# Kernel optimization log

Hardware: AMD Instinct MI355X
Metric: run time of the kernel (lower is better)

The kernel has to match this reference:

```python
import jax, jax.numpy as jnp
import numpy as np

N = 8192      # num nodes = feature dim (A is NxN adjacency used as features)
H = 1024      # bottleneck dim
E = 8192      # num edges
PENALTY = 10.0  # scalar buffer from __init__


def setup_inputs() -> dict:
    key = jax.random.key(0)
    ks = jax.random.split(key, 7)
    return {
        "A": jax.random.normal(ks[0], (N, N), dtype=jnp.float32),
        "W1": jax.random.normal(ks[1], (H, N), dtype=jnp.float32) * 0.02,
        "b1": jax.random.normal(ks[2], (H,), dtype=jnp.float32) * 0.02,
        "W2": jax.random.normal(ks[3], (N, H), dtype=jnp.float32) * 0.02,
        "b2": jax.random.normal(ks[4], (N,), dtype=jnp.float32) * 0.02,
        "edges": jax.random.randint(ks[5], (E, 2), 0, N, dtype=jnp.int32),
        "labels": jax.random.randint(ks[6], (E,), 0, 2, dtype=jnp.int32),
    }


def reference(A, W1, b1, W2, b2, edges, labels):
    ni = edges[:, 0]
    nj = edges[:, 1]
    Xi = A[ni]  # [E, N]
    Xj = A[nj]  # [E, N]
    lab = labels.astype(A.dtype)

    layers = [(W1, b1), (W2, b2)]
    Hi, Hj = Xi, Xj
    loss_1 = jnp.zeros((), A.dtype)
    loss_r_per_edge = jnp.zeros((), A.dtype)
    for (W, b) in layers:
        Hi = jax.nn.sigmoid(Hi @ W.T + b)
        Hj = jax.nn.sigmoid(Hj @ W.T + b)
        # per-edge L2 norm of activation diff at this layer, weighted by label
        loss_1 = loss_1 + jnp.sum(jnp.linalg.norm(Hi - Hj, axis=1) * lab)
        # original code appends weight-row-norm sum + bias norm once per (edge, layer)
        loss_r_per_edge = loss_r_per_edge + jnp.sum(jnp.linalg.norm(W, axis=1)) + jnp.linalg.norm(b)
    loss_r = loss_r_per_edge * jnp.asarray(E, A.dtype)

    # reconstruction loss; penalty scales the diff when label >= 1 (scalar => factors out of norm)
    factor = jnp.where(lab >= 1.0, jnp.asarray(PENALTY, A.dtype), jnp.asarray(1.0, A.dtype))
    loss_2 = jnp.sum(factor * (jnp.linalg.norm(Xi - Hi, axis=1) + jnp.linalg.norm(Xj - Hj, axis=1)))

    return loss_1 + loss_2 + loss_r
```

## Files before the change

### kernel.cpp

```cpp
#include <hip/hip_runtime.h>
#include <hip/hip_bf16.h>
#include <stdint.h>

#define N_DIM 8192
#define H_DIM 1024
#define E_DIM 8192
#define PENALTY_F 10.0f
#define WSCALE 16.0f
#define INV_WSCALE 0.0625f

typedef unsigned short u16;
typedef unsigned char u8;
typedef unsigned int u32;
typedef __attribute__((ext_vector_type(4))) float f32x4;
typedef __attribute__((ext_vector_type(2))) float f32x2;
typedef __attribute__((ext_vector_type(4))) int i32x4;
typedef __attribute__((ext_vector_type(8))) int i32x8;

__device__ __forceinline__ u32 pack4_fp8(float a, float b, float c, float d) {
  u32 p = __builtin_amdgcn_cvt_pk_fp8_f32(a, b, 0, false);
  p = __builtin_amdgcn_cvt_pk_fp8_f32(c, d, p, true);
  return p;
}
__device__ __forceinline__ f32x2 unpk_lo(u32 v) {
  return __builtin_amdgcn_cvt_pk_f32_fp8(v, false);
}
__device__ __forceinline__ f32x2 unpk_hi(u32 v) {
  return __builtin_amdgcn_cvt_pk_f32_fp8(v, true);
}

#define GLD16(ldsptr, gptr)                                                     \
  __builtin_amdgcn_global_load_lds(                                             \
      (__attribute__((address_space(1))) void*)(gptr),                          \
      (__attribute__((address_space(3))) void*)(ldsptr), 16, 0, 0)

__device__ __forceinline__ float wave_red(float v) {
  for (int o = 32; o; o >>= 1) v += __shfl_down(v, o, 64);
  return v;
}

__device__ __forceinline__ float block_reduce1(float v) {
  __shared__ float buf[4];
  v = wave_red(v);
  int lane = threadIdx.x & 63, w = threadIdx.x >> 6;
  if (lane == 0) buf[w] = v;
  __syncthreads();
  float r = 0.f;
  if (threadIdx.x == 0) r = buf[0] + buf[1] + buf[2] + buf[3];
  return r;
}

__global__ void convert_f32_fp8(const float* __restrict__ in,
                                u8* __restrict__ out, int n4, float scale) {
  int i = blockIdx.x * blockDim.x + threadIdx.x;
  if (i < n4) {
    float4 v = ((const float4*)in)[i];
    ((u32*)out)[i] =
        pack4_fp8(v.x * scale, v.y * scale, v.z * scale, v.w * scale);
  }
}

__global__ void prep_w(const float* __restrict__ W1,
                       const float* __restrict__ W2,
                       const float* __restrict__ b1,
                       const float* __restrict__ b2, u8* __restrict__ W1_8,
                       u8* __restrict__ W2_8, float* __restrict__ out) {
  const int blk = blockIdx.x;
  if (blk < H_DIM) {
    const float4* row = (const float4*)(W1 + (size_t)blk * N_DIM);
    u32* orow = (u32*)(W1_8 + (size_t)blk * N_DIM);
    float s = 0.f;
#pragma unroll
    for (int t = 0; t < 8; ++t) {
      int i = threadIdx.x + t * 256;
      float4 v = row[i];
      s += v.x * v.x + v.y * v.y + v.z * v.z + v.w * v.w;
      orow[i] = pack4_fp8(v.x * WSCALE, v.y * WSCALE, v.z * WSCALE,
                          v.w * WSCALE);
    }
    s = block_reduce1(s);
    if (threadIdx.x == 0) atomicAdd(out, sqrtf(s) * (float)E_DIM);
  } else if (blk < H_DIM + N_DIM / 4) {
    __shared__ float buf[4];
    const int wave = threadIdx.x >> 6, lane = threadIdx.x & 63;
    const int r = (blk - H_DIM) * 4 + wave;
    const float4* row = (const float4*)(W2 + (size_t)r * H_DIM);
    u32* orow = (u32*)(W2_8 + (size_t)r * H_DIM);
    float s = 0.f;
#pragma unroll
    for (int t = 0; t < 4; ++t) {
      int i = lane + t * 64;
      float4 v = row[i];
      s += v.x * v.x + v.y * v.y + v.z * v.z + v.w * v.w;
      orow[i] = pack4_fp8(v.x * WSCALE, v.y * WSCALE, v.z * WSCALE,
                          v.w * WSCALE);
    }
    s = wave_red(s);
    if (lane == 0) buf[wave] = sqrtf(s);
    __syncthreads();
    if (threadIdx.x == 0)
      atomicAdd(out, (buf[0] + buf[1] + buf[2] + buf[3]) * (float)E_DIM);
  } else if (blk == H_DIM + N_DIM / 4) {
    const float4* row = (const float4*)b1;
    float4 v = row[threadIdx.x];
    float s = v.x * v.x + v.y * v.y + v.z * v.z + v.w * v.w;
    s = block_reduce1(s);
    if (threadIdx.x == 0) atomicAdd(out, sqrtf(s) * (float)E_DIM);
  } else {
    const float4* row = (const float4*)b2;
    float s = 0.f;
#pragma unroll
    for (int t = 0; t < 8; ++t) {
      float4 v = row[threadIdx.x + t * 256];
      s += v.x * v.x + v.y * v.y + v.z * v.z + v.w * v.w;
    }
    s = block_reduce1(s);
    if (threadIdx.x == 0) atomicAdd(out, sqrtf(s) * (float)E_DIM);
  }
}

#define BM 128
#define BN 128
#define BKB 128

__global__ __launch_bounds__(256) void gemm_fp8_sigmoid(
    const u8* __restrict__ Ag,
    const u8* __restrict__ Bg,
    const float* __restrict__ bias,
    u8* __restrict__ Cg,
    float invScale, int K, int Nd) {
  __shared__ __align__(16) u8 Xs[BM * BKB];
  __shared__ __align__(16) u8 Ws[BN * BKB];

  const int tid = threadIdx.x;
  const int wave = tid >> 6, lane = tid & 63;
  const int wr = wave >> 1, wc = wave & 1;
  const size_t rowBase = (size_t)blockIdx.y * BM;
  const size_t colBase = (size_t)blockIdx.x * BN;

  f32x4 acc[4][4] = {};

  const int i8 = lane >> 3;
  const int c8 = lane & 7;
  const int sw = c8 ^ i8;

  const int quad = lane >> 4;
  const int m15 = lane & 15;

  for (int k0 = 0; k0 < K; k0 += BKB) {
#pragma unroll
    for (int j = 0; j < 4; ++j) {
      const int r0 = (wave * 4 + j) * 8;
      const u8* gx = Ag + (rowBase + r0 + i8) * (size_t)K + (k0 + sw * 16);
      GLD16(&Xs[r0 * BKB], gx);
      const u8* gw = Bg + (colBase + r0 + i8) * (size_t)K + (k0 + sw * 16);
      GLD16(&Ws[r0 * BKB], gw);
    }
    __syncthreads();

    i32x8 af[4], bfr[4];
#pragma unroll
    for (int t = 0; t < 4; ++t) {
      const int m = wr * 64 + t * 16 + m15;
      i32x4 alo = *(const i32x4*)&Xs[m * BKB + ((2 * quad) ^ (m & 7)) * 16];
      i32x4 ahi = *(const i32x4*)&Xs[m * BKB + ((2 * quad + 1) ^ (m & 7)) * 16];
      af[t] = __builtin_shufflevector(alo, ahi, 0, 1, 2, 3, 4, 5, 6, 7);
      const int n = wc * 64 + t * 16 + m15;
      i32x4 blo = *(const i32x4*)&Ws[n * BKB + ((2 * quad) ^ (n & 7)) * 16];
      i32x4 bhi = *(const i32x4*)&Ws[n * BKB + ((2 * quad + 1) ^ (n & 7)) * 16];
      bfr[t] = __builtin_shufflevector(blo, bhi, 0, 1, 2, 3, 4, 5, 6, 7);
    }
#pragma unroll
    for (int mt = 0; mt < 4; ++mt)
#pragma unroll
      for (int nt = 0; nt < 4; ++nt)
        acc[mt][nt] = __builtin_amdgcn_mfma_scale_f32_16x16x128_f8f6f4(
            bfr[nt], af[mt], acc[mt][nt], 0, 0,
            0, 0x7F7F7F7F, 0, 0x7F7F7F7F);
    __syncthreads();
  }

  f32x4 bv4[4];
#pragma unroll
  for (int nt = 0; nt < 4; ++nt)
    bv4[nt] = *(const f32x4*)&bias[colBase + wc * 64 + nt * 16 + quad * 4];
#pragma unroll
  for (int mt = 0; mt < 4; ++mt) {
    const size_t grow = rowBase + wr * 64 + mt * 16 + m15;
    u32* crow = (u32*)(Cg + grow * (size_t)Nd + colBase + wc * 64);
#pragma unroll
    for (int nt = 0; nt < 4; ++nt) {
      float v[4];
#pragma unroll
      for (int i = 0; i < 4; ++i) {
        float x = acc[mt][nt][i] * invScale + bv4[nt][i];
        v[i] = WSCALE / (1.0f + __expf(-x));
      }
      crow[nt * 4 + quad] = pack4_fp8(v[0], v[1], v[2], v[3]);
    }
  }
}

__global__ void edge_loss_h(const u8* __restrict__ H1,
                            const int* __restrict__ edges,
                            const int* __restrict__ labels,
                            float* __restrict__ out) {
  __shared__ float buf[4];
  const int wave = threadIdx.x >> 6, lane = threadIdx.x & 63;
  const int e = blockIdx.x * 4 + wave;
  float r = 0.f;
  if (labels[e] != 0) {
    const int ni = edges[e * 2], nj = edges[e * 2 + 1];
    const i32x4 a = ((const i32x4*)(H1 + (size_t)ni * H_DIM))[lane];
    const i32x4 b = ((const i32x4*)(H1 + (size_t)nj * H_DIM))[lane];
    float s = 0.f;
#pragma unroll
    for (int j = 0; j < 4; ++j) {
      f32x2 al = unpk_lo((u32)a[j]), ah = unpk_hi((u32)a[j]);
      f32x2 bl = unpk_lo((u32)b[j]), bh = unpk_hi((u32)b[j]);
      float d0 = al.x - bl.x, d1 = al.y - bl.y;
      float d2 = ah.x - bh.x, d3 = ah.y - bh.y;
      s += d0 * d0 + d1 * d1 + d2 * d2 + d3 * d3;
    }
    s = wave_red(s);
    r = sqrtf(s) * INV_WSCALE;
  }
  if (lane == 0) buf[wave] = r;
  __syncthreads();
  if (threadIdx.x == 0) atomicAdd(out, buf[0] + buf[1] + buf[2] + buf[3]);
}

__global__ void edge_loss_final(const u8* __restrict__ H2,
                                const u8* __restrict__ A8,
                                const int* __restrict__ edges,
                                const int* __restrict__ labels,
                                float* __restrict__ out) {
  __shared__ float buf[4];
  const int wave = threadIdx.x >> 6, lane = threadIdx.x & 63;
  const int e = blockIdx.x * 4 + wave;
  const int ni = edges[e * 2], nj = edges[e * 2 + 1];
  const i32x4* hi = (const i32x4*)(H2 + (size_t)ni * N_DIM);
  const i32x4* hj = (const i32x4*)(H2 + (size_t)nj * N_DIM);
  const i32x4* xi = (const i32x4*)(A8 + (size_t)ni * N_DIM);
  const i32x4* xj = (const i32x4*)(A8 + (size_t)nj * N_DIM);
  float s12 = 0.f, si = 0.f, sj = 0.f;
#pragma unroll 2
  for (int t = 0; t < 8; ++t) {
    const int idx = lane + t * 64;
    i32x4 a = hi[idx], b = hj[idx], x = xi[idx], y = xj[idx];
#pragma unroll
    for (int j = 0; j < 4; ++j) {
      f32x2 al = unpk_lo((u32)a[j]), ah = unpk_hi((u32)a[j]);
      f32x2 bl = unpk_lo((u32)b[j]), bh = unpk_hi((u32)b[j]);
      f32x2 xl = unpk_lo((u32)x[j]), xh = unpk_hi((u32)x[j]);
      f32x2 yl = unpk_lo((u32)y[j]), yh = unpk_hi((u32)y[j]);
      float d;
      d = al.x - bl.x; s12 += d * d;
      d = al.y - bl.y; s12 += d * d;
      d = ah.x - bh.x; s12 += d * d;
      d = ah.y - bh.y; s12 += d * d;
      d = WSCALE * xl.x - al.x; si += d * d;
      d = WSCALE * xl.y - al.y; si += d * d;
      d = WSCALE * xh.x - ah.x; si += d * d;
      d = WSCALE * xh.y - ah.y; si += d * d;
      d = WSCALE * yl.x - bl.x; sj += d * d;
      d = WSCALE * yl.y - bl.y; sj += d * d;
      d = WSCALE * yh.x - bh.x; sj += d * d;
      d = WSCALE * yh.y - bh.y; sj += d * d;
    }
  }
  for (int o = 32; o; o >>= 1) {
    s12 += __shfl_down(s12, o, 64);
    si += __shfl_down(si, o, 64);
    sj += __shfl_down(sj, o, 64);
  }
  if (lane == 0) {
    float lab = (labels[e] != 0) ? 1.f : 0.f;
    float fac = (labels[e] != 0) ? PENALTY_F : 1.f;
    buf[wave] = (lab * sqrtf(s12) + fac * (sqrtf(si) + sqrtf(sj))) * INV_WSCALE;
  }
  __syncthreads();
  if (threadIdx.x == 0) atomicAdd(out, buf[0] + buf[1] + buf[2] + buf[3]);
}

extern "C" void kernel_launch(void* const* d_in, const int* in_sizes, int n_in,
                              void* d_out, int out_size, void* d_ws,
                              size_t ws_size, hipStream_t stream) {
  const float* A = (const float*)d_in[0];
  const float* W1 = (const float*)d_in[1];
  const float* b1 = (const float*)d_in[2];
  const float* W2 = (const float*)d_in[3];
  const float* b2 = (const float*)d_in[4];
  const int* edges = (const int*)d_in[5];
  const int* labels = (const int*)d_in[6];
  float* out = (float*)d_out;

  char* ws = (char*)d_ws;
  u8* A8   = (u8*)(ws);
  u8* H1_8 = (u8*)(ws + 67108864ull);
  u8* H2_8 = (u8*)(ws + 75497472ull);
  u8* W1_8 = (u8*)(ws + 142606336ull);
  u8* W2_8 = (u8*)(ws + 150994944ull);

  hipMemsetAsync(out, 0, sizeof(float), stream);

  convert_f32_fp8<<<(N_DIM * N_DIM / 4 + 255) / 256, 256, 0, stream>>>(
      A, A8, N_DIM * N_DIM / 4, 1.0f);

  prep_w<<<H_DIM + N_DIM / 4 + 2, 256, 0, stream>>>(W1, W2, b1, b2, W1_8,
                                                    W2_8, out);

  gemm_fp8_sigmoid<<<dim3(H_DIM / BN, N_DIM / BM), 256, 0, stream>>>(
      A8, W1_8, b1, H1_8, INV_WSCALE, N_DIM, H_DIM);
  edge_loss_h<<<E_DIM / 4, 256, 0, stream>>>(H1_8, edges, labels, out);

  gemm_fp8_sigmoid<<<dim3(N_DIM / BN, N_DIM / BM), 256, 0, stream>>>(
      H1_8, W2_8, b2, H2_8, INV_WSCALE * INV_WSCALE, H_DIM, N_DIM);
  edge_loss_final<<<E_DIM / 4, 256, 0, stream>>>(H2_8, A8, edges, labels, out);
}
```

Before: 721.5 us.

## Add 256x256 double-buffered FP8 GEMM for layer 2 and XCD block remap for layer 1

Layer 2's GEMM now uses a new kernel with 256x256 tiles, 512 threads and double-buffered LDS staging, so the next K-tile loads while the current one is multiplied. The first GEMM also remaps block IDs across the eight XCDs so neighbouring tiles share L2. The larger tile raises operand reuse per load but adds register pressure (8x4 accumulators) and shared memory use. The grid shrinks to 32x32 blocks, which may hurt occupancy or tail balance.

```diff
diff --git a/kernel.cpp b/kernel.cpp
--- a/kernel.cpp
+++ b/kernel.cpp
@@ -132,11 +132,17 @@
   __shared__ __align__(16) u8 Xs[BM * BKB];
   __shared__ __align__(16) u8 Ws[BN * BKB];
 
+  const int nwg = gridDim.x * gridDim.y;
+  const int id = blockIdx.y * gridDim.x + blockIdx.x;
+  const int wg = (id & 7) * (nwg >> 3) + (id >> 3);
+  const int bx = wg % gridDim.x;
+  const int by = wg / gridDim.x;
+
   const int tid = threadIdx.x;
   const int wave = tid >> 6, lane = tid & 63;
   const int wr = wave >> 1, wc = wave & 1;
-  const size_t rowBase = (size_t)blockIdx.y * BM;
-  const size_t colBase = (size_t)blockIdx.x * BN;
+  const size_t rowBase = (size_t)by * BM;
+  const size_t colBase = (size_t)bx * BN;
 
   f32x4 acc[4][4] = {};
 
@@ -187,6 +193,99 @@
 #pragma unroll
   for (int mt = 0; mt < 4; ++mt) {
     const size_t grow = rowBase + wr * 64 + mt * 16 + m15;
+    u32* crow = (u32*)(Cg + grow * (size_t)Nd + colBase + wc * 64);
+#pragma unroll
+    for (int nt = 0; nt < 4; ++nt) {
+      float v[4];
+#pragma unroll
+      for (int i = 0; i < 4; ++i) {
+        float x = acc[mt][nt][i] * invScale + bv4[nt][i];
+        v[i] = WSCALE / (1.0f + __expf(-x));
+      }
+      crow[nt * 4 + quad] = pack4_fp8(v[0], v[1], v[2], v[3]);
+    }
+  }
+}
+
+#define BM2 256
+#define BN2 256
+
+__global__ __launch_bounds__(512, 2) void gemm2_fp8_sigmoid(
+    const u8* __restrict__ Ag,
+    const u8* __restrict__ Bg,
+    const float* __restrict__ bias,
+    u8* __restrict__ Cg,
+    float invScale, int K, int Nd) {
+  __shared__ __align__(16) u8 Xs[2][BM2 * BKB];
+  __shared__ __align__(16) u8 Ws[2][BN2 * BKB];
+
+  const int tid = threadIdx.x;
+  const int wave = tid >> 6, lane = tid & 63;
+  const int wr = wave >> 2;
+  const int wc = wave & 3;
+  const size_t rowBase = (size_t)blockIdx.y * BM2;
+  const size_t colBase = (size_t)blockIdx.x * BN2;
+
+  f32x4 acc[8][4] = {};
+
+  const int i8 = lane >> 3;
+  const int c8 = lane & 7;
+  const int sw = c8 ^ i8;
+  const int quad = lane >> 4;
+  const int m15 = lane & 15;
+
+  const int T = K / BKB;
+
+  auto STAGE = [&](int kt, int b) {
+    const size_t kOff = (size_t)kt * BKB + sw * 16;
+#pragma unroll
+    for (int j = 0; j < 4; ++j) {
+      const int r0 = (wave * 4 + j) * 8;
+      GLD16(&Xs[b][r0 * BKB], Ag + (rowBase + r0 + i8) * (size_t)K + kOff);
+      GLD16(&Ws[b][r0 * BKB], Bg + (colBase + r0 + i8) * (size_t)K + kOff);
+    }
+  };
+
+  STAGE(0, 0);
+  __syncthreads();
+
+  for (int t = 0; t < T; ++t) {
+    const int cur = t & 1;
+    if (t + 1 < T) STAGE(t + 1, cur ^ 1);
+
+    const u8* Xb = Xs[cur];
+    const u8* Wb = Ws[cur];
+
+    i32x8 bfr[4];
+#pragma unroll
+    for (int nt = 0; nt < 4; ++nt) {
+      const int n = wc * 64 + nt * 16 + m15;
+      i32x4 blo = *(const i32x4*)&Wb[n * BKB + ((2 * quad) ^ (n & 7)) * 16];
+      i32x4 bhi = *(const i32x4*)&Wb[n * BKB + ((2 * quad + 1) ^ (n & 7)) * 16];
+      bfr[nt] = __builtin_shufflevector(blo, bhi, 0, 1, 2, 3, 4, 5, 6, 7);
+    }
+#pragma unroll
+    for (int mt = 0; mt < 8; ++mt) {
+      const int m = wr * 128 + mt * 16 + m15;
+      i32x4 alo = *(const i32x4*)&Xb[m * BKB + ((2 * quad) ^ (m & 7)) * 16];
+      i32x4 ahi = *(const i32x4*)&Xb[m * BKB + ((2 * quad + 1) ^ (m & 7)) * 16];
+      i32x8 af = __builtin_shufflevector(alo, ahi, 0, 1, 2, 3, 4, 5, 6, 7);
+#pragma unroll
+      for (int nt = 0; nt < 4; ++nt)
+        acc[mt][nt] = __builtin_amdgcn_mfma_scale_f32_16x16x128_f8f6f4(
+            bfr[nt], af, acc[mt][nt], 0, 0,
+            0, 0x7F7F7F7F, 0, 0x7F7F7F7F);
+    }
+    __syncthreads();
+  }
+
+  f32x4 bv4[4];
+#pragma unroll
+  for (int nt = 0; nt < 4; ++nt)
+    bv4[nt] = *(const f32x4*)&bias[colBase + wc * 64 + nt * 16 + quad * 4];
+#pragma unroll
+  for (int mt = 0; mt < 8; ++mt) {
+    const size_t grow = rowBase + wr * 128 + mt * 16 + m15;
     u32* crow = (u32*)(Cg + grow * (size_t)Nd + colBase + wc * 64);
 #pragma unroll
     for (int nt = 0; nt < 4; ++nt) {
@@ -314,7 +413,7 @@
       A8, W1_8, b1, H1_8, INV_WSCALE, N_DIM, H_DIM);
   edge_loss_h<<<E_DIM / 4, 256, 0, stream>>>(H1_8, edges, labels, out);
 
-  gemm_fp8_sigmoid<<<dim3(N_DIM / BN, N_DIM / BM), 256, 0, stream>>>(
+  gemm2_fp8_sigmoid<<<dim3(N_DIM / BN2, N_DIM / BM2), 512, 0, stream>>>(
       H1_8, W2_8, b2, H2_8, INV_WSCALE * INV_WSCALE, H_DIM, N_DIM);
   edge_loss_final<<<E_DIM / 4, 256, 0, stream>>>(H2_8, A8, edges, labels, out);
 }
```

Result: faster. 704.4 us (-2.4%).
